# Kernel optimization log

Hardware: AMD Instinct MI355X
Metric: run time of the kernel (lower is better)

The kernel has to match this reference:

```python
import jax, jax.numpy as jnp
import numpy as np

IN, H, T = 1024, 2048, 2048

def setup_inputs() -> dict:
    key = jax.random.key(0)
    ks = jax.random.split(key, 10)
    x = jax.random.normal(ks[0], (1, T, IN), dtype=jnp.float32)
    # strictly increasing timestamps
    time = jnp.cumsum(jax.random.uniform(ks[1], (T,), dtype=jnp.float32))
    # xavier-ish scaled weights, uniform(0,1) biases as in init_weights
    W_ih = jax.random.normal(ks[2], (4 * H, IN), dtype=jnp.float32) * (1.0 / np.sqrt(IN))
    W_hh = jax.random.normal(ks[3], (4 * H, H), dtype=jnp.float32) * (1.0 / np.sqrt(H))
    b_ih = jax.random.uniform(ks[4], (4 * H,), dtype=jnp.float32)
    b_hh = jax.random.uniform(ks[5], (4 * H,), dtype=jnp.float32)
    decay_w = jax.random.normal(ks[6], (H,), dtype=jnp.float32)
    decay_b = jax.random.uniform(ks[7], (H,), dtype=jnp.float32)
    h0 = jax.random.normal(ks[8], (1, H), dtype=jnp.float32) * 0.1
    c0 = jax.random.normal(ks[9], (1, H), dtype=jnp.float32) * 0.1
    return {"x": x, "time": time, "W_ih": W_ih, "W_hh": W_hh, "b_ih": b_ih,
            "b_hh": b_hh, "decay_w": decay_w, "decay_b": decay_b, "h0": h0, "c0": c0}


def reference(x, time, W_ih, W_hh, b_ih, b_hh, decay_w, decay_b, h0, c0):
    Tn = x.shape[1]
    Hn = h0.shape[1]
    # dt[i] = time[i] - time[i-1], dt[0] = 0
    dt = jnp.concatenate([jnp.zeros((1,), x.dtype), time[1:] - time[:-1]])
    # step i (i>0) decays h with gamma(dt[i-1]); step 0 uses gamma = 1
    dt_prev = jnp.concatenate([jnp.zeros((1,), x.dtype), dt[:-1]])  # [T]
    gamma = jnp.exp(-jax.nn.relu(dt_prev[:, None] * decay_w[None, :] + decay_b[None, :]))  # [T,H]
    gamma = jnp.where((jnp.arange(Tn) > 0)[:, None], gamma, jnp.ones((), x.dtype))
    # precompute input contribution for all steps: [T, 4H]
    xg = x[0] @ W_ih.T + b_ih + b_hh

    def step(carry, inp):
        h, c = carry  # [H], [H]
        xg_t, gamma_t = inp
        h = h * gamma_t
        gates = xg_t + h @ W_hh.T  # [4H]
        i_, f_, g_, o_ = jnp.split(gates, 4)
        i_ = jax.nn.sigmoid(i_)
        f_ = jax.nn.sigmoid(f_)
        g_ = jnp.tanh(g_)
        o_ = jax.nn.sigmoid(o_)
        c = f_ * c + i_ * g_
        h = o_ * jnp.tanh(c)
        return (h, c), h

    (h_f, c_f), hs = jax.lax.scan(step, (h0[0], c0[0]), (xg, gamma))  # hs: [T,H]
    # dot-product attention pooling against final hidden state
    attn = hs @ h_f  # [T]
    w = jax.nn.softmax(attn)
    context = w @ hs  # [H]
    return context[None, :]  # [1, H]
```

## Files before the change

kernel.cpp:

```cpp
#include <hip/hip_runtime.h>
#include <hip/hip_bf16.h>

#define H 2048
#define T 2048
#define INPUT 1024
#define FOURH 8192
#define NBLK 256
#define RING 512

typedef __attribute__((ext_vector_type(8))) short bf16x8;
typedef __attribute__((ext_vector_type(4))) float f32x4_t;

__device__ __forceinline__ unsigned short f2bf(float f) {
  union { float f; unsigned u; } v; v.f = f;
  unsigned r = v.u + 0x7FFFu + ((v.u >> 16) & 1u);
  return (unsigned short)(r >> 16);
}

__global__ void prep_kernel(const float* __restrict__ x, const float* __restrict__ W_ih,
                            const float* __restrict__ time_, short* __restrict__ xb,
                            short* __restrict__ wb, float* __restrict__ dtp,
                            unsigned* __restrict__ flags) {
  size_t i = (size_t)blockIdx.x * blockDim.x + threadIdx.x;
  size_t stride = (size_t)gridDim.x * blockDim.x;
  if (i < (size_t)T * INPUT) xb[i] = (short)f2bf(x[i]);
  for (size_t j = i; j < (size_t)FOURH * INPUT; j += stride) wb[j] = (short)f2bf(W_ih[j]);
  if (i < T) dtp[i] = (i >= 2) ? (time_[i - 1] - time_[i - 2]) : 0.0f;
  if (i < NBLK) flags[i] = 0u;
}

__global__ void __launch_bounds__(256)
gemm_xg(const short* __restrict__ A, const short* __restrict__ B,
        const float* __restrict__ b_ih, const float* __restrict__ b_hh,
        float* __restrict__ xg) {
  int wave = threadIdx.x >> 6;
  int lane = threadIdx.x & 63;
  int m0 = blockIdx.y << 4;
  int n0 = (blockIdx.x << 6) + (wave << 4);
  int r16 = lane & 15, q = lane >> 4;
  const short* ap = A + (size_t)(m0 + r16) * INPUT + q * 8;
  const short* bp = B + (size_t)(n0 + r16) * INPUT + q * 8;
  f32x4_t acc = {0.f, 0.f, 0.f, 0.f};
#pragma unroll 4
  for (int k = 0; k < INPUT; k += 32) {
    bf16x8 av = *(const bf16x8*)(ap + k);
    bf16x8 bv = *(const bf16x8*)(bp + k);
    acc = __builtin_amdgcn_mfma_f32_16x16x32_bf16(av, bv, acc, 0, 0, 0);
  }
  int n = n0 + r16;
  float bias = b_ih[n] + b_hh[n];
#pragma unroll
  for (int r = 0; r < 4; ++r) {
    int m = m0 + q * 4 + r;
    xg[(size_t)m * FOURH + n] = acc[r] + bias;
  }
}

__device__ __forceinline__ void epoch_bar(unsigned* flags, unsigned e) {
  __syncthreads();
  if (threadIdx.x == 0)
    __hip_atomic_store(&flags[blockIdx.x], e, __ATOMIC_RELEASE, __HIP_MEMORY_SCOPE_AGENT);
  if (threadIdx.x < NBLK) {
    while (__hip_atomic_load(&flags[threadIdx.x], __ATOMIC_RELAXED,
                             __HIP_MEMORY_SCOPE_AGENT) < e) {
    }
  }
  __builtin_amdgcn_fence(__ATOMIC_ACQUIRE, "agent");
  __syncthreads();
}

__global__ void __launch_bounds__(512, 2)
lstm_rec(const float* __restrict__ xg, const float* __restrict__ W_hh,
         const float* __restrict__ decay_w, const float* __restrict__ decay_b,
         const float* __restrict__ h0, const float* __restrict__ c0,
         const float* __restrict__ dtp, float* __restrict__ hs,
         unsigned* ring, unsigned* flags) {
  const int wave = threadIdx.x >> 6;
  const int lane = threadIdx.x & 63;
  const int u = (blockIdx.x << 3) + wave;
  __shared__ __align__(16) float lh[H];

  float wreg[4][32];
#pragma unroll
  for (int g = 0; g < 4; ++g) {
    const float* wr = W_hh + (size_t)(g * H + u) * H + lane;
#pragma unroll
    for (int j = 0; j < 32; ++j) wreg[g][j] = wr[(size_t)j << 6];
  }
  const float dw = decay_w[u], db = decay_b[u];
  float c = c0[u];
  if (lane == 0) {
    unsigned pk = (1u << 16) | (unsigned)f2bf(h0[u]);
    __hip_atomic_store(&ring[u], pk, __ATOMIC_RELAXED, __HIP_MEMORY_SCOPE_AGENT);
  }

  for (int t = 0; t < T; ++t) {
    if ((t & 255) == 0 && t) epoch_bar(flags, (unsigned)(t >> 8));

    float xi = 0.f, xf = 0.f, xgv = 0.f, xo = 0.f, dtn = 0.f;
    if (lane == 0) {
      const float* xr = xg + (size_t)t * FOURH;
      xi = xr[u]; xf = xr[H + u]; xgv = xr[2 * H + u]; xo = xr[3 * H + u];
      if (t + 1 < T) dtn = dtp[t + 1];
    }

    const unsigned want = (unsigned)t + 1u;
    const int wbase = (wave << 8) + (lane << 2);
    unsigned long long* sp = (unsigned long long*)(
        ring + (((size_t)(t & (RING - 1)) << 11) | (unsigned)wbase));
    unsigned long long w0, w1;
    for (;;) {
      w0 = __hip_atomic_load(sp,     __ATOMIC_RELAXED, __HIP_MEMORY_SCOPE_AGENT);
      w1 = __hip_atomic_load(sp + 1, __ATOMIC_RELAXED, __HIP_MEMORY_SCOPE_AGENT);
      unsigned t0 = ((unsigned)w0) >> 16;
      unsigned t1 = (unsigned)(w0 >> 48);
      unsigned t2 = ((unsigned)w1) >> 16;
      unsigned t3 = (unsigned)(w1 >> 48);
      int bad = (t0 != want) | (t1 != want) | (t2 != want) | (t3 != want);
      if (!__any(bad)) break;
    }
    {
      f32x4_t hv;
      union { unsigned u; float f; } v;
      v.u = ((unsigned)w0 & 0xFFFFu) << 16;          hv.x = v.f;
      v.u = ((unsigned)(w0 >> 32) & 0xFFFFu) << 16;  hv.y = v.f;
      v.u = ((unsigned)w1 & 0xFFFFu) << 16;          hv.z = v.f;
      v.u = ((unsigned)(w1 >> 32) & 0xFFFFu) << 16;  hv.w = v.f;
      *(f32x4_t*)&lh[wbase] = hv;
    }
    __syncthreads();

    float a0 = 0.f, a1 = 0.f, a2 = 0.f, a3 = 0.f;
#pragma unroll
    for (int j = 0; j < 32; ++j) {
      float h = lh[(j << 6) + lane];
      a0 += wreg[0][j] * h;
      a1 += wreg[1][j] * h;
      a2 += wreg[2][j] * h;
      a3 += wreg[3][j] * h;
    }
#pragma unroll
    for (int s = 32; s >= 1; s >>= 1) {
      a0 += __shfl_xor(a0, s);
      a1 += __shfl_xor(a1, s);
      a2 += __shfl_xor(a2, s);
      a3 += __shfl_xor(a3, s);
    }
    if (lane == 0) {
      float iv = a0 + xi;
      float fv = a1 + xf;
      float gv = a2 + xgv;
      float ov = a3 + xo;
      iv = 1.f / (1.f + __expf(-iv));
      fv = 1.f / (1.f + __expf(-fv));
      gv = tanhf(gv);
      ov = 1.f / (1.f + __expf(-ov));
      c = fv * c + iv * gv;
      float h = ov * tanhf(c);
      hs[(size_t)t * H + u] = h;
      if (t + 1 < T) {
        float gam = __expf(-fmaxf(0.f, dtn * dw + db));
        unsigned pk = (((unsigned)(t + 2)) << 16) | (unsigned)f2bf(h * gam);
        size_t slot = (size_t)((t + 1) & (RING - 1)) << 11;
        __hip_atomic_store(&ring[slot | (unsigned)u], pk, __ATOMIC_RELAXED,
                           __HIP_MEMORY_SCOPE_AGENT);
      }
    }
    __syncthreads();
  }
}

__global__ void attn_k(const float* __restrict__ hs, float* __restrict__ attn) {
  int t = blockIdx.x;
  const float* row = hs + (size_t)t * H;
  const float* hf = hs + (size_t)(T - 1) * H;
  float s = 0.f;
  for (int i = threadIdx.x; i < H; i += 256) s += row[i] * hf[i];
#pragma unroll
  for (int o = 32; o; o >>= 1) s += __shfl_down(s, o);
  __shared__ float wsum[4];
  if ((threadIdx.x & 63) == 0) wsum[threadIdx.x >> 6] = s;
  __syncthreads();
  if (threadIdx.x == 0) attn[t] = wsum[0] + wsum[1] + wsum[2] + wsum[3];
}

__global__ void softmax_k(float* __restrict__ a) {
  int tid = threadIdx.x;
  __shared__ float red[16];
  __shared__ float bcast;
  float m = -1e30f;
  for (int i = tid; i < T; i += 1024) m = fmaxf(m, a[i]);
#pragma unroll
  for (int o = 32; o; o >>= 1) m = fmaxf(m, __shfl_xor(m, o));
  if ((tid & 63) == 0) red[tid >> 6] = m;
  __syncthreads();
  if (tid == 0) {
    float mm = red[0];
    for (int i = 1; i < 16; ++i) mm = fmaxf(mm, red[i]);
    bcast = mm;
  }
  __syncthreads();
  float M = bcast, s = 0.f;
  for (int i = tid; i < T; i += 1024) { float e = __expf(a[i] - M); a[i] = e; s += e; }
#pragma unroll
  for (int o = 32; o; o >>= 1) s += __shfl_xor(s, o);
  if ((tid & 63) == 0) red[tid >> 6] = s;
  __syncthreads();
  if (tid == 0) {
    float ss = 0.f;
    for (int i = 0; i < 16; ++i) ss += red[i];
    bcast = 1.f / ss;
  }
  __syncthreads();
  float inv = bcast;
  for (int i = tid; i < T; i += 1024) a[i] *= inv;
}

__global__ void ctx_k(const float* __restrict__ hs, const float* __restrict__ w,
                      float* __restrict__ out) {
  int h = (blockIdx.x << 8) + threadIdx.x;
  int t0 = blockIdx.y << 6;
  float acc = 0.f;
  for (int t = t0; t < t0 + 64; ++t) acc += w[t] * hs[(size_t)t * H + h];
  atomicAdd(&out[h], acc);
}

extern "C" void kernel_launch(void* const* d_in, const int* in_sizes, int n_in,
                              void* d_out, int out_size, void* d_ws, size_t ws_size,
                              hipStream_t stream) {
  const float* x       = (const float*)d_in[0];
  const float* time_   = (const float*)d_in[1];
  const float* W_ih    = (const float*)d_in[2];
  const float* W_hh    = (const float*)d_in[3];
  const float* b_ih    = (const float*)d_in[4];
  const float* b_hh    = (const float*)d_in[5];
  const float* decay_w = (const float*)d_in[6];
  const float* decay_b = (const float*)d_in[7];
  const float* h0      = (const float*)d_in[8];
  const float* c0      = (const float*)d_in[9];

  char* ws = (char*)d_ws;
  float*    xg   = (float*)ws;
  float*    hs   = (float*)(ws + (64u << 20));
  short*    xb   = (short*)(ws + (80u << 20));
  short*    wb   = (short*)(ws + (84u << 20));
  unsigned* ring = (unsigned*)(ws + (100u << 20));
  float*    dtp  = (float*)(ws + (108u << 20));
  float*    attn = dtp + T;
  unsigned* flags = (unsigned*)(attn + T);

  prep_kernel<<<8192, 256, 0, stream>>>(x, W_ih, time_, xb, wb, dtp, flags);

  dim3 g1(FOURH / 64, T / 16);
  gemm_xg<<<g1, 256, 0, stream>>>(xb, wb, b_ih, b_hh, xg);

  {
    void* args[] = {&xg, (void*)&W_hh, (void*)&decay_w, (void*)&decay_b,
                    (void*)&h0, (void*)&c0, &dtp, &hs, &ring, &flags};
    (void)hipLaunchCooperativeKernel((void*)lstm_rec, dim3(NBLK), dim3(512), args, 0, stream);
  }

  attn_k<<<T, 256, 0, stream>>>(hs, attn);
  softmax_k<<<1, 1024, 0, stream>>>(attn);
  (void)hipMemsetAsync(d_out, 0, out_size * sizeof(float), stream);
  ctx_k<<<dim3(H / 256, T / 64), 256, 0, stream>>>(hs, attn, (float*)d_out);
}
```

Baseline: 7.123 ms.

## Double-buffer LSTM hidden-state LDS to drop a barrier and vectorize loads

The recurrent kernel now keeps two LDS buffers for the hidden state, alternating by step parity, which lets it remove the second __syncthreads per timestep. W_hh rows are loaded and consumed as float4 so each lane reads four contiguous hidden values per LDS load. The decay factor is computed before the spin-wait instead of on the critical path after the gates, and the hs store is moved after the ring publish. The xg GEMM grid is flattened to 1D with the M index varying fastest, which changes the block order to improve B reuse in cache. Dropping the barrier depends on the ring-flag spin to keep one buffer from being overwritten while another wave is still reading it.

```diff
diff --git a/kernel.cpp b/kernel.cpp
--- a/kernel.cpp
+++ b/kernel.cpp
@@ -35,8 +35,9 @@
         float* __restrict__ xg) {
   int wave = threadIdx.x >> 6;
   int lane = threadIdx.x & 63;
-  int m0 = blockIdx.y << 4;
-  int n0 = (blockIdx.x << 6) + (wave << 4);
+  int bid = blockIdx.x;
+  int m0 = (bid & 127) << 4;
+  int n0 = ((bid >> 7) << 6) + (wave << 4);
   int r16 = lane & 15, q = lane >> 4;
   const short* ap = A + (size_t)(m0 + r16) * INPUT + q * 8;
   const short* bp = B + (size_t)(n0 + r16) * INPUT + q * 8;
@@ -78,14 +79,15 @@
   const int wave = threadIdx.x >> 6;
   const int lane = threadIdx.x & 63;
   const int u = (blockIdx.x << 3) + wave;
-  __shared__ __align__(16) float lh[H];
+  __shared__ __align__(16) float lh[2][H];
 
   float wreg[4][32];
 #pragma unroll
   for (int g = 0; g < 4; ++g) {
-    const float* wr = W_hh + (size_t)(g * H + u) * H + lane;
-#pragma unroll
-    for (int j = 0; j < 32; ++j) wreg[g][j] = wr[(size_t)j << 6];
+    const float* wr = W_hh + (size_t)(g * H + u) * H + (lane << 2);
+#pragma unroll
+    for (int p = 0; p < 8; ++p)
+      *(f32x4_t*)&wreg[g][p << 2] = *(const f32x4_t*)(wr + (p << 8));
   }
   const float dw = decay_w[u], db = decay_b[u];
   float c = c0[u];
@@ -97,11 +99,11 @@
   for (int t = 0; t < T; ++t) {
     if ((t & 255) == 0 && t) epoch_bar(flags, (unsigned)(t >> 8));
 
-    float xi = 0.f, xf = 0.f, xgv = 0.f, xo = 0.f, dtn = 0.f;
+    float xi = 0.f, xf = 0.f, xgv = 0.f, xo = 0.f, gam = 0.f;
     if (lane == 0) {
       const float* xr = xg + (size_t)t * FOURH;
       xi = xr[u]; xf = xr[H + u]; xgv = xr[2 * H + u]; xo = xr[3 * H + u];
-      if (t + 1 < T) dtn = dtp[t + 1];
+      if (t + 1 < T) gam = __expf(-fmaxf(0.f, dtp[t + 1] * dw + db));
     }
 
     const unsigned want = (unsigned)t + 1u;
@@ -119,6 +121,7 @@
       int bad = (t0 != want) | (t1 != want) | (t2 != want) | (t3 != want);
       if (!__any(bad)) break;
     }
+    float* lb = lh[t & 1];
     {
       f32x4_t hv;
       union { unsigned u; float f; } v;
@@ -126,18 +129,22 @@
       v.u = ((unsigned)(w0 >> 32) & 0xFFFFu) << 16;  hv.y = v.f;
       v.u = ((unsigned)w1 & 0xFFFFu) << 16;          hv.z = v.f;
       v.u = ((unsigned)(w1 >> 32) & 0xFFFFu) << 16;  hv.w = v.f;
-      *(f32x4_t*)&lh[wbase] = hv;
+      *(f32x4_t*)(lb + wbase) = hv;
     }
     __syncthreads();
 
     float a0 = 0.f, a1 = 0.f, a2 = 0.f, a3 = 0.f;
 #pragma unroll
-    for (int j = 0; j < 32; ++j) {
-      float h = lh[(j << 6) + lane];
-      a0 += wreg[0][j] * h;
-      a1 += wreg[1][j] * h;
-      a2 += wreg[2][j] * h;
-      a3 += wreg[3][j] * h;
+    for (int p = 0; p < 8; ++p) {
+      f32x4_t h4 = *(const f32x4_t*)(lb + (p << 8) + (lane << 2));
+#pragma unroll
+      for (int e = 0; e < 4; ++e) {
+        float h = h4[e];
+        a0 += wreg[0][(p << 2) + e] * h;
+        a1 += wreg[1][(p << 2) + e] * h;
+        a2 += wreg[2][(p << 2) + e] * h;
+        a3 += wreg[3][(p << 2) + e] * h;
+      }
     }
 #pragma unroll
     for (int s = 32; s >= 1; s >>= 1) {
@@ -157,16 +164,14 @@
       ov = 1.f / (1.f + __expf(-ov));
       c = fv * c + iv * gv;
       float h = ov * tanhf(c);
-      hs[(size_t)t * H + u] = h;
       if (t + 1 < T) {
-        float gam = __expf(-fmaxf(0.f, dtn * dw + db));
         unsigned pk = (((unsigned)(t + 2)) << 16) | (unsigned)f2bf(h * gam);
         size_t slot = (size_t)((t + 1) & (RING - 1)) << 11;
         __hip_atomic_store(&ring[slot | (unsigned)u], pk, __ATOMIC_RELAXED,
                            __HIP_MEMORY_SCOPE_AGENT);
       }
-    }
-    __syncthreads();
+      hs[(size_t)t * H + u] = h;
+    }
   }
 }
 
@@ -251,8 +256,7 @@
 
   prep_kernel<<<8192, 256, 0, stream>>>(x, W_ih, time_, xb, wb, dtp, flags);
 
-  dim3 g1(FOURH / 64, T / 16);
-  gemm_xg<<<g1, 256, 0, stream>>>(xb, wb, b_ih, b_hh, xg);
+  gemm_xg<<<16384, 256, 0, stream>>>(xb, wb, b_ih, b_hh, xg);
 
   {
     void* args[] = {&xg, (void*)&W_hh, (void*)&decay_w, (void*)&decay_b,
```

After: 12.21 ms. 71.5% more time.
